# Kernel optimization log

Hardware: AMD Instinct MI355X
Metric: run time of the kernel (lower is better)

## Reference

```python
import jax, jax.numpy as jnp
import numpy as np

B, S, D, O, R, E = 4, 2048, 4096, 4096, 16, 8
SCALING = 32.0 / 16.0  # lora_alpha / lora_rank


def setup_inputs() -> dict:
    key = jax.random.key(0)
    ks = jax.random.split(key, 7)
    x = jax.random.normal(ks[0], (B, S, D), dtype=jnp.float32)
    W_base = jax.random.normal(ks[1], (O, D), dtype=jnp.float32) * 0.02
    b_base = jnp.zeros((O,), dtype=jnp.float32)
    A_w = jax.random.normal(ks[2], (R, D), dtype=jnp.float32) * 0.02     # lora_A weight
    B_w = jax.random.normal(ks[3], (O, R), dtype=jnp.float32) * 0.02     # lora_B weight
    router_w = jax.random.normal(ks[4], (E, D), dtype=jnp.float32) * 0.02  # router weight (core_router=False -> acts on x)
    cores = jax.random.normal(ks[5], (E, R, R), dtype=jnp.float32)       # expert rank x rank cores
    return {"x": x, "W_base": W_base, "b_base": b_base, "A_w": A_w,
            "B_w": B_w, "router_w": router_w, "cores": cores}


def reference(x, W_base, b_base, A_w, B_w, router_w, cores):
    # base linear: [B,S,O]
    result = jnp.einsum('bsd,od->bso', x, W_base) + b_base
    # lora down-projection (dropout=0 -> identity): [B,S,R]
    ax = jnp.einsum('bsd,rd->bsr', x, A_w)
    # router on x (core_router=False): softmax over experts -> [B,S,E]
    probs = jax.nn.softmax(jnp.einsum('bsd,ed->bse', x, router_w), axis=-1)
    # per-token weighted core applied to ax WITHOUT materializing [B,S,R,R]:
    # first ax through each expert core [B,S,E,R], then weight-reduce over experts.
    per_expert = jnp.einsum('bsr,erq->bseq', ax, cores)
    mixed = jnp.einsum('bseq,bse->bsq', per_expert, probs)  # [B,S,R]
    result = result + jnp.einsum('bsr,or->bso', mixed, B_w) * SCALING
    return result
```

## Files before the change

kernel.cpp:

```cpp
#include <hip/hip_runtime.h>
#include <stdint.h>

#define D_DIM 4096
#define O_DIM 4096
#define M_DIM 8192
#define BK 32
#define NKT 128

typedef __attribute__((ext_vector_type(4))) float f32x4;
typedef __attribute__((ext_vector_type(8))) __bf16 bf16x8;
typedef __attribute__((ext_vector_type(8))) unsigned short u16x8;

__device__ __forceinline__ unsigned short f32_to_bf16_bits(float f) {
    union { float f; uint32_t u; } v; v.f = f;
    return (unsigned short)((v.u + 0x7FFFu + ((v.u >> 16) & 1u)) >> 16);
}

__device__ __forceinline__ float dot4(f32x4 a, f32x4 b) {
    return fmaf(a.x, b.x, fmaf(a.y, b.y, fmaf(a.z, b.z, a.w * b.w)));
}

__device__ __forceinline__ int swz(int b) { return b ^ (((b >> 7) & 7) << 4); }

__global__ __launch_bounds__(256) void convert_bf16_kernel(const float* __restrict__ src,
                                                           unsigned short* __restrict__ dst,
                                                           int n4) {
    int stride = gridDim.x * blockDim.x;
    for (int i = blockIdx.x * blockDim.x + threadIdx.x; i < n4; i += stride) {
        f32x4 v = ((const f32x4*)src)[i];
        ushort4 o;
        o.x = f32_to_bf16_bits(v.x);
        o.y = f32_to_bf16_bits(v.y);
        o.z = f32_to_bf16_bits(v.z);
        o.w = f32_to_bf16_bits(v.w);
        ((ushort4*)dst)[i] = o;
    }
}

__global__ __launch_bounds__(256) void partial_mixed_kernel(const float* __restrict__ x,
                                                            const float* __restrict__ A_w,
                                                            const float* __restrict__ router_w,
                                                            unsigned short* __restrict__ xbf,
                                                            float* __restrict__ ypart) {
    __shared__ __align__(16) float Xc[32][132];
    __shared__ __align__(16) float Wc[24][132];

    const int tid = threadIdx.x;
    const int t0 = blockIdx.x * 32;
    const int d0 = blockIdx.y * 512;

    const int slot = tid & 63;
    const int q = tid >> 6;
    const int tg4 = slot >> 3;
    const int og = slot & 7;

    float acc[4][3];
    #pragma unroll
    for (int ti = 0; ti < 4; ++ti)
        #pragma unroll
        for (int wi = 0; wi < 3; ++wi) acc[ti][wi] = 0.f;

    for (int sub = 0; sub < 4; ++sub) {
        const int dbase = d0 + sub * 128;
        __syncthreads();
        #pragma unroll
        for (int i = 0; i < 4; ++i) {
            int idx = i * 256 + tid;
            int t = idx >> 5, dq = idx & 31;
            f32x4 v = *(const f32x4*)&x[(size_t)(t0 + t) * D_DIM + dbase + dq * 4];
            *(f32x4*)&Xc[t][dq * 4] = v;
            ushort4 o;
            o.x = f32_to_bf16_bits(v.x);
            o.y = f32_to_bf16_bits(v.y);
            o.z = f32_to_bf16_bits(v.z);
            o.w = f32_to_bf16_bits(v.w);
            *(ushort4*)&xbf[(size_t)(t0 + t) * D_DIM + dbase + dq * 4] = o;
        }
        #pragma unroll
        for (int i = 0; i < 3; ++i) {
            int idx = i * 256 + tid;
            int r = idx >> 5, dq = idx & 31;
            const float* src = (r < 16) ? (A_w + (size_t)r * D_DIM)
                                        : (router_w + (size_t)(r - 16) * D_DIM);
            *(f32x4*)&Wc[r][dq * 4] = *(const f32x4*)&src[dbase + dq * 4];
        }
        __syncthreads();
        #pragma unroll
        for (int dqi = 0; dqi < 8; ++dqi) {
            const int dq = q * 8 + dqi;
            f32x4 w0 = *(const f32x4*)&Wc[og * 3 + 0][dq * 4];
            f32x4 w1 = *(const f32x4*)&Wc[og * 3 + 1][dq * 4];
            f32x4 w2 = *(const f32x4*)&Wc[og * 3 + 2][dq * 4];
            #pragma unroll
            for (int ti = 0; ti < 4; ++ti) {
                f32x4 xv = *(const f32x4*)&Xc[tg4 * 4 + ti][dq * 4];
                acc[ti][0] += dot4(xv, w0);
                acc[ti][1] += dot4(xv, w1);
                acc[ti][2] += dot4(xv, w2);
            }
        }
    }

    __syncthreads();
    float* red = &Xc[0][0];
    #pragma unroll
    for (int ti = 0; ti < 4; ++ti)
        #pragma unroll
        for (int wi = 0; wi < 3; ++wi)
            red[(slot * 4 + q) * 12 + ti * 3 + wi] = acc[ti][wi];
    __syncthreads();
    #pragma unroll
    for (int k = 0; k < 3; ++k) {
        const int flat = tid * 3 + k;
        const int t = flat / 24, j = flat % 24;
        const int s = ((t >> 2) << 3) | (j / 3);
        const int ti = t & 3, wi = j % 3;
        float v = 0.f;
        #pragma unroll
        for (int qq = 0; qq < 4; ++qq) v += red[(s * 4 + qq) * 12 + ti * 3 + wi];
        ypart[(((size_t)blockIdx.y * 256 + blockIdx.x) * 32 + t) * 24 + j] = v;
    }
}

__global__ __launch_bounds__(128) void fin_kernel(const float* __restrict__ ypart,
                                                  const float* __restrict__ cores,
                                                  const float* __restrict__ Bw,
                                                  unsigned short* __restrict__ mixbf,
                                                  unsigned short* __restrict__ bwbf) {
    const int tid = threadIdx.x;

    if (blockIdx.x >= 64) {
        const int o = (blockIdx.x - 64) * 128 + tid;
        ushort4* dst = (ushort4*)&bwbf[(size_t)o * 32];
        #pragma unroll
        for (int g = 0; g < 4; ++g) {
            f32x4 v = *(const f32x4*)&Bw[(size_t)o * 16 + g * 4];
            ushort4 u;
            u.x = f32_to_bf16_bits(v.x);
            u.y = f32_to_bf16_bits(v.y);
            u.z = f32_to_bf16_bits(v.z);
            u.w = f32_to_bf16_bits(v.w);
            dst[g] = u;
        }
        const ushort4 z = {0, 0, 0, 0};
        #pragma unroll
        for (int g = 4; g < 8; ++g) dst[g] = z;
        return;
    }

    __shared__ __align__(16) float Cs[2048];
    #pragma unroll
    for (int i = 0; i < 4; ++i) {
        int idx = i * 128 + tid;
        ((f32x4*)Cs)[idx] = ((const f32x4*)cores)[idx];
    }
    __syncthreads();

    const int tok = blockIdx.x * 128 + tid;
    const int tile = tok >> 5, t = tok & 31;

    float y[24];
    #pragma unroll
    for (int j = 0; j < 24; ++j) y[j] = 0.f;
    for (int ds = 0; ds < 8; ++ds) {
        const float* src = ypart + (((size_t)ds * 256 + tile) * 32 + t) * 24;
        #pragma unroll
        for (int j = 0; j < 24; ++j) y[j] += src[j];
    }

    float mx = y[16];
    #pragma unroll
    for (int e = 1; e < 8; ++e) mx = fmaxf(mx, y[16 + e]);
    float p[8], psum = 0.f;
    #pragma unroll
    for (int e = 0; e < 8; ++e) { p[e] = __expf(y[16 + e] - mx); psum += p[e]; }
    const float inv = 1.0f / psum;

    float outq[16];
    #pragma unroll
    for (int q = 0; q < 16; ++q) outq[q] = 0.f;
    for (int e = 0; e < 8; ++e) {
        const float pe = p[e] * inv;
        #pragma unroll
        for (int r = 0; r < 16; ++r) {
            const float ar = y[r] * pe;
            #pragma unroll
            for (int q = 0; q < 16; ++q)
                outq[q] = fmaf(ar, Cs[(e * 16 + r) * 16 + q], outq[q]);
        }
    }
    ushort4* dst = (ushort4*)&mixbf[(size_t)tok * 32];
    #pragma unroll
    for (int g = 0; g < 4; ++g) {
        ushort4 u;
        u.x = f32_to_bf16_bits(2.0f * outq[g * 4 + 0]);
        u.y = f32_to_bf16_bits(2.0f * outq[g * 4 + 1]);
        u.z = f32_to_bf16_bits(2.0f * outq[g * 4 + 2]);
        u.w = f32_to_bf16_bits(2.0f * outq[g * 4 + 3]);
        dst[g] = u;
    }
    const ushort4 z = {0, 0, 0, 0};
    #pragma unroll
    for (int g = 4; g < 8; ++g) dst[g] = z;
}

__global__ __launch_bounds__(512, 2) void gemm_kernel(const unsigned short* __restrict__ xbf,
                                                      const unsigned short* __restrict__ wbf,
                                                      const float* __restrict__ bias,
                                                      const unsigned short* __restrict__ mixbf,
                                                      const unsigned short* __restrict__ bwbf,
                                                      float* __restrict__ out) {
    __shared__ __align__(16) unsigned short lds[4][2][256 * 32];

    const int bid = blockIdx.x;
    const int xcd = bid & 7;
    const int lid = bid >> 3;
    const int tm = (lid >> 4) * 8 + xcd;
    const int tn = lid & 15;
    const int m0 = tm * 256, n0 = tn * 256;

    const int tid = threadIdx.x;
    const int wave = tid >> 6, lane = tid & 63;
    const int wr = wave >> 2, wcn = wave & 3;

    int aoff[2], boff[2], mmoff[2], mboff[2];
    #pragma unroll
    for (int u = 0; u < 2; ++u) {
        int c = u * 512 + tid;
        int g = swz(c * 16);
        int grow = g >> 6, gc8 = (g >> 4) & 3;
        aoff[u] = (m0 + grow) * D_DIM + gc8 * 8;
        boff[u] = (n0 + grow) * D_DIM + gc8 * 8;
        mmoff[u] = (m0 + grow) * 32 + gc8 * 8;
        mboff[u] = (n0 + grow) * 32 + gc8 * 8;
    }

    const int tA = lane & 15, kq = lane >> 4;
    int aRd[8], bRd[4];
    #pragma unroll
    for (int mi = 0; mi < 8; ++mi)
        aRd[mi] = swz((wr * 128 + mi * 16 + tA) * 64 + kq * 16);
    #pragma unroll
    for (int ni = 0; ni < 4; ++ni)
        bRd[ni] = swz((wcn * 64 + ni * 16 + tA) * 64 + kq * 16);

    f32x4 acc[8][4];
    const f32x4 fz = {0.f, 0.f, 0.f, 0.f};
    #pragma unroll
    for (int mi = 0; mi < 8; ++mi)
        #pragma unroll
        for (int ni = 0; ni < 4; ++ni) acc[mi][ni] = fz;

#define STAGE_UNIT(sb, kt, u, isA)                                                        \
    do {                                                                                  \
        const unsigned short* gsrc =                                                      \
            (isA) ? (xbf + aoff[u] + (kt)*BK) : (wbf + boff[u] + (kt)*BK);                \
        __builtin_amdgcn_global_load_lds(                                                 \
            (const __attribute__((address_space(1))) void*)gsrc,                          \
            (__attribute__((address_space(3))) void*)(&lds[sb][(isA) ? 0 : 1]             \
                                                         [((u)*512 + wave * 64) * 8]),    \
            16, 0, 0);                                                                    \
    } while (0)

#define STAGE_MIX(u, isA)                                                                 \
    do {                                                                                  \
        const unsigned short* gsrc = (isA) ? (mixbf + mmoff[u]) : (bwbf + mboff[u]);      \
        __builtin_amdgcn_global_load_lds(                                                 \
            (const __attribute__((address_space(1))) void*)gsrc,                          \
            (__attribute__((address_space(3))) void*)(&lds[0][(isA) ? 0 : 1]              \
                                                         [((u)*512 + wave * 64) * 8]),    \
            16, 0, 0);                                                                    \
    } while (0)

#define K_ITER(BUF, SBUF, KT, STG, VMC)                                                   \
    {                                                                                     \
        const char* Ab = (const char*)&lds[BUF][0][0];                                    \
        const char* Bb = (const char*)&lds[BUF][1][0];                                    \
        bf16x8 b0 = __builtin_bit_cast(bf16x8, *(const u16x8*)(Bb + bRd[0]));             \
        bf16x8 b1 = __builtin_bit_cast(bf16x8, *(const u16x8*)(Bb + bRd[1]));             \
        bf16x8 b2 = __builtin_bit_cast(bf16x8, *(const u16x8*)(Bb + bRd[2]));             \
        bf16x8 b3 = __builtin_bit_cast(bf16x8, *(const u16x8*)(Bb + bRd[3]));             \
        bf16x8 a0 = __builtin_bit_cast(bf16x8, *(const u16x8*)(Ab + aRd[0]));             \
        bf16x8 a1 = __builtin_bit_cast(bf16x8, *(const u16x8*)(Ab + aRd[1]));             \
        bf16x8 a2 = __builtin_bit_cast(bf16x8, *(const u16x8*)(Ab + aRd[2]));             \
        bf16x8 a3 = __builtin_bit_cast(bf16x8, *(const u16x8*)(Ab + aRd[3]));             \
        if (STG) {                                                                        \
            STAGE_UNIT(SBUF, KT, 0, 1);                                                   \
            STAGE_UNIT(SBUF, KT, 1, 1);                                                   \
        }                                                                                 \
        asm volatile("" ::: "memory");                                                    \
        __builtin_amdgcn_s_barrier();                                                     \
        asm volatile("" ::: "memory");                                                    \
        __builtin_amdgcn_s_setprio(1);                                                    \
        acc[0][0] = __builtin_amdgcn_mfma_f32_16x16x32_bf16(a0, b0, acc[0][0], 0, 0, 0);  \
        acc[0][1] = __builtin_amdgcn_mfma_f32_16x16x32_bf16(a0, b1, acc[0][1], 0, 0, 0);  \
        acc[0][2] = __builtin_amdgcn_mfma_f32_16x16x32_bf16(a0, b2, acc[0][2], 0, 0, 0);  \
        acc[0][3] = __builtin_amdgcn_mfma_f32_16x16x32_bf16(a0, b3, acc[0][3], 0, 0, 0);  \
        acc[1][0] = __builtin_amdgcn_mfma_f32_16x16x32_bf16(a1, b0, acc[1][0], 0, 0, 0);  \
        acc[1][1] = __builtin_amdgcn_mfma_f32_16x16x32_bf16(a1, b1, acc[1][1], 0, 0, 0);  \
        acc[1][2] = __builtin_amdgcn_mfma_f32_16x16x32_bf16(a1, b2, acc[1][2], 0, 0, 0);  \
        acc[1][3] = __builtin_amdgcn_mfma_f32_16x16x32_bf16(a1, b3, acc[1][3], 0, 0, 0);  \
        acc[2][0] = __builtin_amdgcn_mfma_f32_16x16x32_bf16(a2, b0, acc[2][0], 0, 0, 0);  \
        acc[2][1] = __builtin_amdgcn_mfma_f32_16x16x32_bf16(a2, b1, acc[2][1], 0, 0, 0);  \
        acc[2][2] = __builtin_amdgcn_mfma_f32_16x16x32_bf16(a2, b2, acc[2][2], 0, 0, 0);  \
        acc[2][3] = __builtin_amdgcn_mfma_f32_16x16x32_bf16(a2, b3, acc[2][3], 0, 0, 0);  \
        acc[3][0] = __builtin_amdgcn_mfma_f32_16x16x32_bf16(a3, b0, acc[3][0], 0, 0, 0);  \
        acc[3][1] = __builtin_amdgcn_mfma_f32_16x16x32_bf16(a3, b1, acc[3][1], 0, 0, 0);  \
        acc[3][2] = __builtin_amdgcn_mfma_f32_16x16x32_bf16(a3, b2, acc[3][2], 0, 0, 0);  \
        acc[3][3] = __builtin_amdgcn_mfma_f32_16x16x32_bf16(a3, b3, acc[3][3], 0, 0, 0);  \
        __builtin_amdgcn_s_setprio(0);                                                    \
        asm volatile("" ::: "memory");                                                    \
        __builtin_amdgcn_s_barrier();                                                     \
        asm volatile("" ::: "memory");                                                    \
        bf16x8 a4 = __builtin_bit_cast(bf16x8, *(const u16x8*)(Ab + aRd[4]));             \
        bf16x8 a5 = __builtin_bit_cast(bf16x8, *(const u16x8*)(Ab + aRd[5]));             \
        bf16x8 a6 = __builtin_bit_cast(bf16x8, *(const u16x8*)(Ab + aRd[6]));             \
        bf16x8 a7 = __builtin_bit_cast(bf16x8, *(const u16x8*)(Ab + aRd[7]));             \
        if (STG) {                                                                        \
            STAGE_UNIT(SBUF, KT, 0, 0);                                                   \
            STAGE_UNIT(SBUF, KT, 1, 0);                                                   \
        }                                                                                 \
        asm volatile("s_waitcnt vmcnt(" #VMC ")" ::: "memory");                           \
        __builtin_amdgcn_s_barrier();                                                     \
        asm volatile("" ::: "memory");                                                    \
        __builtin_amdgcn_s_setprio(1);                                                    \
        acc[4][0] = __builtin_amdgcn_mfma_f32_16x16x32_bf16(a4, b0, acc[4][0], 0, 0, 0);  \
        acc[4][1] = __builtin_amdgcn_mfma_f32_16x16x32_bf16(a4, b1, acc[4][1], 0, 0, 0);  \
        acc[4][2] = __builtin_amdgcn_mfma_f32_16x16x32_bf16(a4, b2, acc[4][2], 0, 0, 0);  \
        acc[4][3] = __builtin_amdgcn_mfma_f32_16x16x32_bf16(a4, b3, acc[4][3], 0, 0, 0);  \
        acc[5][0] = __builtin_amdgcn_mfma_f32_16x16x32_bf16(a5, b0, acc[5][0], 0, 0, 0);  \
        acc[5][1] = __builtin_amdgcn_mfma_f32_16x16x32_bf16(a5, b1, acc[5][1], 0, 0, 0);  \
        acc[5][2] = __builtin_amdgcn_mfma_f32_16x16x32_bf16(a5, b2, acc[5][2], 0, 0, 0);  \
        acc[5][3] = __builtin_amdgcn_mfma_f32_16x16x32_bf16(a5, b3, acc[5][3], 0, 0, 0);  \
        acc[6][0] = __builtin_amdgcn_mfma_f32_16x16x32_bf16(a6, b0, acc[6][0], 0, 0, 0);  \
        acc[6][1] = __builtin_amdgcn_mfma_f32_16x16x32_bf16(a6, b1, acc[6][1], 0, 0, 0);  \
        acc[6][2] = __builtin_amdgcn_mfma_f32_16x16x32_bf16(a6, b2, acc[6][2], 0, 0, 0);  \
        acc[6][3] = __builtin_amdgcn_mfma_f32_16x16x32_bf16(a6, b3, acc[6][3], 0, 0, 0);  \
        acc[7][0] = __builtin_amdgcn_mfma_f32_16x16x32_bf16(a7, b0, acc[7][0], 0, 0, 0);  \
        acc[7][1] = __builtin_amdgcn_mfma_f32_16x16x32_bf16(a7, b1, acc[7][1], 0, 0, 0);  \
        acc[7][2] = __builtin_amdgcn_mfma_f32_16x16x32_bf16(a7, b2, acc[7][2], 0, 0, 0);  \
        acc[7][3] = __builtin_amdgcn_mfma_f32_16x16x32_bf16(a7, b3, acc[7][3], 0, 0, 0);  \
        __builtin_amdgcn_s_setprio(0);                                                    \
        asm volatile("s_waitcnt lgkmcnt(0)" ::: "memory");                                \
        __builtin_amdgcn_s_barrier();                                                     \
        asm volatile("" ::: "memory");                                                    \
    }

    #pragma unroll
    for (int kt = 0; kt < 3; ++kt) {
        STAGE_UNIT(kt, kt, 0, 1);
        STAGE_UNIT(kt, kt, 1, 1);
        STAGE_UNIT(kt, kt, 0, 0);
        STAGE_UNIT(kt, kt, 1, 0);
    }
    asm volatile("s_waitcnt vmcnt(8)" ::: "memory");
    __builtin_amdgcn_s_barrier();
    asm volatile("" ::: "memory");

    for (int jj = 0; jj < 31; ++jj) {
        #pragma unroll
        for (int i = 0; i < 4; ++i) {
            const int j = jj * 4 + i;
            const int kt = j + 3;
            K_ITER(i, (i + 3) & 3, kt, 1, 8);
        }
    }
    K_ITER(0, 3, 127, 1, 8);
    K_ITER(1, 0, 0, 0, 4);
    K_ITER(2, 0, 0, 0, 0);
    K_ITER(3, 0, 0, 0, 0);

    STAGE_MIX(0, 1);
    STAGE_MIX(1, 1);
    STAGE_MIX(0, 0);
    STAGE_MIX(1, 0);
    asm volatile("s_waitcnt vmcnt(0)" ::: "memory");
    __builtin_amdgcn_s_barrier();
    asm volatile("" ::: "memory");
    K_ITER(0, 0, 0, 0, 0);
#undef K_ITER
#undef STAGE_MIX
#undef STAGE_UNIT

    const int colq = lane & 15, rq = lane >> 4;
    float bcol[4];
    #pragma unroll
    for (int ni = 0; ni < 4; ++ni) bcol[ni] = bias[n0 + wcn * 64 + ni * 16 + colq];
    #pragma unroll
    for (int mi = 0; mi < 8; ++mi) {
        #pragma unroll
        for (int j = 0; j < 4; ++j) {
            const int row = m0 + wr * 128 + mi * 16 + rq * 4 + j;
            #pragma unroll
            for (int ni = 0; ni < 4; ++ni) {
                const int col = n0 + wcn * 64 + ni * 16 + colq;
                out[(size_t)row * O_DIM + col] = acc[mi][ni][j] + bcol[ni];
            }
        }
    }
}

extern "C" void kernel_launch(void* const* d_in, const int* in_sizes, int n_in,
                              void* d_out, int out_size, void* d_ws, size_t ws_size,
                              hipStream_t stream) {
    const float* x        = (const float*)d_in[0];
    const float* W_base   = (const float*)d_in[1];
    const float* b_base   = (const float*)d_in[2];
    const float* A_w      = (const float*)d_in[3];
    const float* B_w      = (const float*)d_in[4];
    const float* router_w = (const float*)d_in[5];
    const float* cores    = (const float*)d_in[6];
    float* out = (float*)d_out;

    char* ws = (char*)d_ws;
    unsigned short* xbf = (unsigned short*)ws;
    unsigned short* wbf = (unsigned short*)(ws + (size_t)M_DIM * D_DIM * 2);
    char* p = ws + (size_t)M_DIM * D_DIM * 2 + (size_t)O_DIM * D_DIM * 2;
    unsigned short* mixbf = (unsigned short*)p;
    unsigned short* bwbf  = (unsigned short*)(p + (size_t)M_DIM * 32 * 2);
    float* ypart = (float*)(p + (size_t)M_DIM * 32 * 2 + (size_t)O_DIM * 32 * 2);

    convert_bf16_kernel<<<2048, 256, 0, stream>>>(W_base, wbf, (O_DIM * D_DIM) / 4);
    partial_mixed_kernel<<<dim3(256, 8), 256, 0, stream>>>(x, A_w, router_w, xbf, ypart);
    fin_kernel<<<96, 128, 0, stream>>>(ypart, cores, B_w, mixbf, bwbf);
    gemm_kernel<<<512, 512, 0, stream>>>(xbf, wbf, b_base, mixbf, bwbf, out);
}
```

Before: 325.8 us.

## Switch GEMM main loop from 4-stage to 2-stage LDS double buffering

Cuts the LDS ring from four stages to two, halving shared memory from 128KB to 64KB per block. Prefetch distance drops from three tiles to one, and each iteration now waits for all outstanding global loads (vmcnt(0)) at its end. The likely aim is more resident blocks or less LDS pressure, at the cost of less latency hiding for global loads. With launch_bounds(512,2) and the halved LDS, occupancy may not change while memory latency becomes more exposed.

Result: slower. 346.8 us (+6.4%).

```diff
diff --git a/kernel.cpp b/kernel.cpp
--- a/kernel.cpp
+++ b/kernel.cpp
@@ -210,7 +210,7 @@
                                                       const unsigned short* __restrict__ mixbf,
                                                       const unsigned short* __restrict__ bwbf,
                                                       float* __restrict__ out) {
-    __shared__ __align__(16) unsigned short lds[4][2][256 * 32];
+    __shared__ __align__(16) unsigned short lds[2][2][256 * 32];
 
     const int bid = blockIdx.x;
     const int xcd = bid & 7;
@@ -272,7 +272,7 @@
             16, 0, 0);                                                                    \
     } while (0)
 
-#define K_ITER(BUF, SBUF, KT, STG, VMC)                                                   \
+#define K_ITER(BUF, SBUF, KT, STG)                                                        \
     {                                                                                     \
         const char* Ab = (const char*)&lds[BUF][0][0];                                    \
         const char* Bb = (const char*)&lds[BUF][1][0];                                    \
@@ -320,7 +320,7 @@
             STAGE_UNIT(SBUF, KT, 0, 0);                                                   \
             STAGE_UNIT(SBUF, KT, 1, 0);                                                   \
         }                                                                                 \
-        asm volatile("s_waitcnt vmcnt(" #VMC ")" ::: "memory");                           \
+        asm volatile("" ::: "memory");                                                    \
         __builtin_amdgcn_s_barrier();                                                     \
         asm volatile("" ::: "memory");                                                    \
         __builtin_amdgcn_s_setprio(1);                                                    \
@@ -341,34 +341,27 @@
         acc[7][2] = __builtin_amdgcn_mfma_f32_16x16x32_bf16(a7, b2, acc[7][2], 0, 0, 0);  \
         acc[7][3] = __builtin_amdgcn_mfma_f32_16x16x32_bf16(a7, b3, acc[7][3], 0, 0, 0);  \
         __builtin_amdgcn_s_setprio(0);                                                    \
+        if (STG) asm volatile("s_waitcnt vmcnt(0)" ::: "memory");                         \
         asm volatile("s_waitcnt lgkmcnt(0)" ::: "memory");                                \
         __builtin_amdgcn_s_barrier();                                                     \
         asm volatile("" ::: "memory");                                                    \
     }
 
-    #pragma unroll
-    for (int kt = 0; kt < 3; ++kt) {
-        STAGE_UNIT(kt, kt, 0, 1);
-        STAGE_UNIT(kt, kt, 1, 1);
-        STAGE_UNIT(kt, kt, 0, 0);
-        STAGE_UNIT(kt, kt, 1, 0);
-    }
-    asm volatile("s_waitcnt vmcnt(8)" ::: "memory");
+    STAGE_UNIT(0, 0, 0, 1);
+    STAGE_UNIT(0, 0, 1, 1);
+    STAGE_UNIT(0, 0, 0, 0);
+    STAGE_UNIT(0, 0, 1, 0);
+    asm volatile("s_waitcnt vmcnt(0)" ::: "memory");
     __builtin_amdgcn_s_barrier();
     asm volatile("" ::: "memory");
 
-    for (int jj = 0; jj < 31; ++jj) {
-        #pragma unroll
-        for (int i = 0; i < 4; ++i) {
-            const int j = jj * 4 + i;
-            const int kt = j + 3;
-            K_ITER(i, (i + 3) & 3, kt, 1, 8);
-        }
-    }
-    K_ITER(0, 3, 127, 1, 8);
-    K_ITER(1, 0, 0, 0, 4);
-    K_ITER(2, 0, 0, 0, 0);
-    K_ITER(3, 0, 0, 0, 0);
+    for (int jj = 0; jj < 63; ++jj) {
+        const int j = jj * 2;
+        K_ITER(0, 1, j + 1, 1);
+        K_ITER(1, 0, j + 2, 1);
+    }
+    K_ITER(0, 1, 127, 1);
+    K_ITER(1, 0, 0, 0);
 
     STAGE_MIX(0, 1);
     STAGE_MIX(1, 1);
@@ -377,7 +370,7 @@
     asm volatile("s_waitcnt vmcnt(0)" ::: "memory");
     __builtin_amdgcn_s_barrier();
     asm volatile("" ::: "memory");
-    K_ITER(0, 0, 0, 0, 0);
+    K_ITER(0, 1, 0, 0);
 #undef K_ITER
 #undef STAGE_MIX
 #undef STAGE_UNIT
```
